# Kernel optimization log

Measured on AMD Instinct MI355X. Metric: run time of the kernel, lower is better.

## Reference

```python
import jax, jax.numpy as jnp
import numpy as np

DT = 0.01
OMEGA_MAX = 100.0


def setup_inputs() -> dict:
    key = jax.random.key(0)
    ks = jax.random.split(key, 7)
    B, T, D, M = 4, 4096, 1024, 64
    N = 2 * M
    u = jax.random.normal(ks[0], (B, T, D), dtype=jnp.float32)
    W_omega = jax.random.normal(ks[1], (M, D), dtype=jnp.float32) * 0.02
    b_omega = jnp.ones((M,), dtype=jnp.float32)
    W_zeta = jax.random.normal(ks[2], (M, D), dtype=jnp.float32) * 0.02
    b_zeta = jnp.zeros((M,), dtype=jnp.float32)
    W_B = jax.random.normal(ks[3], (N, D), dtype=jnp.float32) * (0.1 / np.sqrt(D))
    b_B = jnp.zeros((N,), dtype=jnp.float32)
    C = jax.random.normal(ks[4], (D, N), dtype=jnp.float32) * 0.01
    D_mat = jax.random.normal(ks[5], (D, D), dtype=jnp.float32) * 0.01
    return dict(u=u, W_omega=W_omega, b_omega=b_omega, W_zeta=W_zeta,
                b_zeta=b_zeta, W_B=W_B, b_B=b_B, C=C, D_mat=D_mat)


def reference(u, W_omega, b_omega, W_zeta, b_zeta, W_B, b_B, C, D_mat):
    B, T, D = u.shape
    M = W_omega.shape[0]
    # Hoist all per-step linear projections into batched GEMMs (same math).
    omega = jax.nn.softplus(jnp.einsum('btd,md->btm', u, W_omega) + b_omega)
    omega = jnp.clip(omega, 1e-4, OMEGA_MAX)                      # (B,T,M)
    zeta = jax.nn.sigmoid(jnp.einsum('btd,md->btm', u, W_zeta) + b_zeta)
    A = omega * omega                                             # (B,T,M)
    S = 1.0 / (1.0 + (DT * DT) * A)                               # (B,T,M)
    d = 1.0 - zeta                                                # (B,T,M)
    F = jnp.einsum('btd,nd->btn', u, W_B) + b_B                   # (B,T,2M)

    def step(x, inp):
        A_t, S_t, d_t, F_t = inp                                  # (B,M)x3, (B,2M)
        z = x[:, :M]
        y = x[:, M:]
        z_new = d_t * (S_t * z - DT * A_t * S_t * y)
        y_new = d_t * (DT * S_t * z + S_t * y)
        x_new = jnp.concatenate([z_new, y_new], axis=-1) + F_t
        return x_new, x_new

    x0 = jnp.zeros((B, 2 * M), dtype=u.dtype)
    tm = lambda a: jnp.swapaxes(a, 0, 1)  # to time-major for scan
    _, xs = jax.lax.scan(step, x0, (tm(A), tm(S), tm(d), tm(F)))
    xs = jnp.swapaxes(xs, 0, 1)                                   # (B,T,2M)
    # Output projection: y_t = x_t C^T + u_t D^T
    y = jnp.einsum('btn,dn->btd', xs, C) + jnp.einsum('bte,de->btd', u, D_mat)
    return y
```

## Files before the change

kernel.cpp:

```cpp
#include <hip/hip_runtime.h>
#include <hip/hip_bf16.h>
#include <math.h>

#define DTC 0.01f

typedef __attribute__((ext_vector_type(8))) short short8;
typedef __attribute__((ext_vector_type(4))) float f32x4;
typedef unsigned short bf16raw;

__device__ __forceinline__ bf16raw f2bf(float f){
  union { unsigned u; float f; } v; v.f = f;
  unsigned r = v.u + 0x7FFF + ((v.u >> 16) & 1u);
  return (bf16raw)(r >> 16);
}

__device__ __forceinline__ short8 ld8f(const float* __restrict__ p){
  float4 a = *(const float4*)p;
  float4 b = *(const float4*)(p + 4);
  short8 r;
  r[0] = (short)f2bf(a.x); r[1] = (short)f2bf(a.y);
  r[2] = (short)f2bf(a.z); r[3] = (short)f2bf(a.w);
  r[4] = (short)f2bf(b.x); r[5] = (short)f2bf(b.y);
  r[6] = (short)f2bf(b.z); r[7] = (short)f2bf(b.w);
  return r;
}

template<int ITERS>
__device__ __forceinline__ void stage_async(const bf16raw* __restrict__ src, long ld,
                                            long row0, int k0, bf16raw* lds,
                                            int wave, int lane){
#pragma unroll
  for (int i = 0; i < ITERS; ++i){
    int r0 = (wave*ITERS + i) * 16;
    long row = row0 + r0 + (lane >> 2);
    const bf16raw* gp = src + row*ld + k0 + (lane & 3)*8;
    bf16raw* lp = lds + r0*32;
    __builtin_amdgcn_global_load_lds((const __attribute__((address_space(1))) void*)gp,
                                     (__attribute__((address_space(3))) void*)lp,
                                     16, 0, 0);
  }
}

template<int NI>
__device__ __forceinline__ void mma_tile(const bf16raw* Alds, const bf16raw* Blds,
                                         f32x4 acc[4][NI], int wm, int wn, int quad, int t16){
  short8 af[4], bfr[NI];
#pragma unroll
  for (int mi = 0; mi < 4; ++mi)
    af[mi] = *(const short8*)(Alds + (wm*64 + mi*16 + t16)*32 + quad*8);
#pragma unroll
  for (int ni = 0; ni < NI; ++ni)
    bfr[ni] = *(const short8*)(Blds + (wn*(NI*16) + ni*16 + t16)*32 + quad*8);
#pragma unroll
  for (int mi = 0; mi < 4; ++mi)
#pragma unroll
    for (int ni = 0; ni < NI; ++ni)
      acc[mi][ni] = __builtin_amdgcn_mfma_f32_16x16x32_bf16(af[mi], bfr[ni], acc[mi][ni], 0, 0, 0);
}

extern "C" __global__ void k_prep(const float* __restrict__ u,
    const float* __restrict__ Wom, const float* __restrict__ Wze,
    const float* __restrict__ WB, const float* __restrict__ Cm,
    const float* __restrict__ Dm, bf16raw* __restrict__ u_bf,
    bf16raw* __restrict__ Wcat, bf16raw* __restrict__ C_bf,
    bf16raw* __restrict__ Dm_bf){
  long g = (long)blockIdx.x * 256 + threadIdx.x;
  const float* src; bf16raw* dst; long o;
  if      (g < 2097152){ src = u;   dst = u_bf;          o = g; }
  else if (g < 2105344){ src = Wom; dst = Wcat;          o = g - 2097152; }
  else if (g < 2113536){ src = Wze; dst = Wcat + 65536;  o = g - 2105344; }
  else if (g < 2129920){ src = WB;  dst = Wcat + 131072; o = g - 2113536; }
  else if (g < 2146304){ src = Cm;  dst = C_bf;          o = g - 2129920; }
  else                 { src = Dm;  dst = Dm_bf;         o = g - 2146304; }
  *(short8*)(dst + o*8) = ld8f(src + o*8);
}

extern "C" __global__ __launch_bounds__(256) void k_gemm_p(
    const bf16raw* __restrict__ u_bf, const bf16raw* __restrict__ Wcat,
    float* __restrict__ P){
  __shared__ __align__(16) bf16raw Alds[128*32];
  __shared__ __align__(16) bf16raw Blds[128*32];
  int tid = threadIdx.x, wave = tid >> 6, lane = tid & 63;
  int quad = lane >> 4, t16 = lane & 15;
  int wm = wave >> 1, wn = wave & 1;
  long row0 = (long)blockIdx.y * 128;
  int  col0 = blockIdx.x * 128;
  f32x4 acc[4][4] = {};
  for (int kt = 0; kt < 32; ++kt){
    __syncthreads();
    stage_async<2>(u_bf, 1024, row0, kt*32, Alds, wave, lane);
    stage_async<2>(Wcat, 1024, col0, kt*32, Blds, wave, lane);
    __syncthreads();
    mma_tile<4>(Alds, Blds, acc, wm, wn, quad, t16);
  }
#pragma unroll
  for (int mi = 0; mi < 4; ++mi)
#pragma unroll
    for (int ni = 0; ni < 4; ++ni)
#pragma unroll
      for (int r = 0; r < 4; ++r){
        long grow = row0 + wm*64 + mi*16 + quad*4 + r;
        int  gcol = col0 + wn*64 + ni*16 + t16;
        P[grow*256 + gcol] = acc[mi][ni][r];
      }
}

extern "C" __global__ __launch_bounds__(256, 2) void k_gemm_out(
    const bf16raw* __restrict__ Xs, const bf16raw* __restrict__ u_bf,
    const bf16raw* __restrict__ C_bf, const bf16raw* __restrict__ Dm_bf,
    float* __restrict__ out){
  __shared__ __align__(16) bf16raw Alds[128*32];
  __shared__ __align__(16) bf16raw Blds[256*32];
  int tid = threadIdx.x, wave = tid >> 6, lane = tid & 63;
  int quad = lane >> 4, t16 = lane & 15;
  int wm = wave >> 1, wn = wave & 1;
  long row0 = (long)blockIdx.y * 128;
  int  col0 = blockIdx.x * 256;
  f32x4 acc[4][8] = {};
  for (int kt = 0; kt < 4; ++kt){
    __syncthreads();
    stage_async<2>(Xs,   128, row0, kt*32, Alds, wave, lane);
    stage_async<4>(C_bf, 128, col0, kt*32, Blds, wave, lane);
    __syncthreads();
    mma_tile<8>(Alds, Blds, acc, wm, wn, quad, t16);
  }
  for (int kt = 0; kt < 32; ++kt){
    __syncthreads();
    stage_async<2>(u_bf,  1024, row0, kt*32, Alds, wave, lane);
    stage_async<4>(Dm_bf, 1024, col0, kt*32, Blds, wave, lane);
    __syncthreads();
    mma_tile<8>(Alds, Blds, acc, wm, wn, quad, t16);
  }
#pragma unroll
  for (int mi = 0; mi < 4; ++mi)
#pragma unroll
    for (int ni = 0; ni < 8; ++ni)
#pragma unroll
      for (int r = 0; r < 4; ++r){
        long grow = row0 + wm*64 + mi*16 + quad*4 + r;
        int  gcol = col0 + wn*128 + ni*16 + t16;
        out[grow*1024 + gcol] = acc[mi][ni][r];
      }
}

extern "C" __global__ void k_coef(const float* __restrict__ P,
    const float* __restrict__ b_om, const float* __restrict__ b_ze,
    const float* __restrict__ b_B, float4* __restrict__ Coef){
  int idx = blockIdx.x * 256 + threadIdx.x;
  int bt = idx >> 6, m = idx & 63;
  const float* row = P + (size_t)bt * 256;
  float wo = row[m]       + b_om[m];
  float wz = row[64 + m]  + b_ze[m];
  float fz = row[128 + m] + b_B[m];
  float fy = row[192 + m] + b_B[64 + m];
  float sp = (wo > 20.f) ? wo : log1pf(expf(wo));
  float omega = fminf(fmaxf(sp, 1e-4f), 100.f);
  float A = omega * omega;
  float S = 1.f / (1.f + DTC*DTC*A);
  float zeta = 1.f / (1.f + expf(-wz));
  float d = 1.f - zeta;
  float p = d * S;
  float q = p * DTC * A;
  Coef[idx] = make_float4(p, q, fz, fy);
}

extern "C" __global__ void k_scan1(const float4* __restrict__ Coef,
    float4* __restrict__ CM, float2* __restrict__ CV){
  int tid = threadIdx.x, c = blockIdx.x;
  int b = tid >> 6, m = tid & 63;
  const float4* cf = Coef + ((size_t)b*4096 + c*32)*64 + m;
  float m00=1.f, m01=0.f, m10=0.f, m11=0.f, vz=0.f, vy=0.f;
#pragma unroll 4
  for (int t = 0; t < 32; ++t){
    float4 f = cf[t*64];
    float p = f.x, q = f.y;
    float nvz = p*vz - q*vy + f.z;
    float nvy = DTC*p*vz + p*vy + f.w;
    vz = nvz; vy = nvy;
    float n00 = p*m00 - q*m10;
    float n01 = p*m01 - q*m11;
    float n10 = DTC*p*m00 + p*m10;
    float n11 = DTC*p*m01 + p*m11;
    m00=n00; m01=n01; m10=n10; m11=n11;
  }
  CM[c*256 + tid] = make_float4(m00, m01, m10, m11);
  CV[c*256 + tid] = make_float2(vz, vy);
}

extern "C" __global__ void k_scan2(const float4* __restrict__ CM,
    const float2* __restrict__ CV, float2* __restrict__ XIn){
  int tid = threadIdx.x;
  float xz = 0.f, xy = 0.f;
#pragma unroll 4
  for (int c = 0; c < 128; ++c){
    XIn[c*256 + tid] = make_float2(xz, xy);
    float4 Mv = CM[c*256 + tid];
    float2 Vv = CV[c*256 + tid];
    float nz = Mv.x*xz + Mv.y*xy + Vv.x;
    float ny = Mv.z*xz + Mv.w*xy + Vv.y;
    xz = nz; xy = ny;
  }
}

extern "C" __global__ void k_scan3(const float4* __restrict__ Coef,
    const float2* __restrict__ XIn, bf16raw* __restrict__ Xs){
  int tid = threadIdx.x, c = blockIdx.x;
  int b = tid >> 6, m = tid & 63;
  const float4* cf = Coef + ((size_t)b*4096 + c*32)*64 + m;
  float2 x0 = XIn[c*256 + tid];
  float xz = x0.x, xy = x0.y;
  bf16raw* xp = Xs + ((size_t)b*4096 + c*32)*128 + m;
#pragma unroll 4
  for (int t = 0; t < 32; ++t){
    float4 f = cf[t*64];
    float p = f.x, q = f.y;
    float nz = p*xz - q*xy + f.z;
    float ny = DTC*p*xz + p*xy + f.w;
    xz = nz; xy = ny;
    xp[t*128]      = f2bf(xz);
    xp[t*128 + 64] = f2bf(xy);
  }
}

extern "C" void kernel_launch(void* const* d_in, const int* in_sizes, int n_in,
                              void* d_out, int out_size, void* d_ws, size_t ws_size,
                              hipStream_t stream){
  const float* u   = (const float*)d_in[0];
  const float* Wom = (const float*)d_in[1];
  const float* bom = (const float*)d_in[2];
  const float* Wze = (const float*)d_in[3];
  const float* bze = (const float*)d_in[4];
  const float* WB  = (const float*)d_in[5];
  const float* bB  = (const float*)d_in[6];
  const float* Cm  = (const float*)d_in[7];
  const float* Dm  = (const float*)d_in[8];
  float* out = (float*)d_out;

  char* ws = (char*)d_ws;
  size_t off = 0;
  bf16raw* u_bf  = (bf16raw*)(ws + off); off += (size_t)16777216*2;
  bf16raw* Wcat  = (bf16raw*)(ws + off); off += (size_t)262144*2;
  bf16raw* C_bf  = (bf16raw*)(ws + off); off += (size_t)131072*2;
  bf16raw* Dm_bf = (bf16raw*)(ws + off); off += (size_t)1048576*2;
  float*   P     = (float*)  (ws + off);
  bf16raw* Xs    = (bf16raw*)P;
  off += (size_t)16384*256*4;
  float4*  Coef  = (float4*) (ws + off); off += (size_t)16384*64*16;
  float4*  CMw   = (float4*) (ws + off); off += (size_t)128*256*16;
  float2*  CVw   = (float2*) (ws + off); off += (size_t)128*256*8;
  float2*  XIn   = (float2*) (ws + off); off += (size_t)128*256*8;

  k_prep    <<<8896, 256, 0, stream>>>(u, Wom, Wze, WB, Cm, Dm, u_bf, Wcat, C_bf, Dm_bf);
  k_gemm_p  <<<dim3(2, 128), 256, 0, stream>>>(u_bf, Wcat, P);
  k_coef    <<<4096, 256, 0, stream>>>(P, bom, bze, bB, Coef);
  k_scan1   <<<128, 256, 0, stream>>>(Coef, CMw, CVw);
  k_scan2   <<<1, 256, 0, stream>>>(CMw, CVw, XIn);
  k_scan3   <<<128, 256, 0, stream>>>(Coef, XIn, Xs);
  k_gemm_out<<<dim3(4, 128), 256, 0, stream>>>(Xs, u_bf, C_bf, Dm_bf, out);
}
```

Baseline: 236.3 us.

## Double-buffer GEMM LDS tiles, swizzle block order, fuse coef into scan and drop serial carry

Both GEMMs now double-buffer their LDS tiles, prefetching the next K slice while the current one is multiplied, and raise wave priority around the MFMA work. Blocks are remapped in a grouped order to improve L2 reuse. The coefficient kernel is fused into the first scan pass, chunk size drops to 16 steps to give 256 blocks, and the single-block carry scan is removed. Each block of the final pass instead recomputes its starting state from all earlier chunk summaries, so the serial launch goes away at the cost of redundant work that grows with chunk index.

```diff
diff --git a/kernel.cpp b/kernel.cpp
--- a/kernel.cpp
+++ b/kernel.cpp
@@ -78,21 +78,35 @@
 extern "C" __global__ __launch_bounds__(256) void k_gemm_p(
     const bf16raw* __restrict__ u_bf, const bf16raw* __restrict__ Wcat,
     float* __restrict__ P){
-  __shared__ __align__(16) bf16raw Alds[128*32];
-  __shared__ __align__(16) bf16raw Blds[128*32];
+  __shared__ __align__(16) bf16raw Alds[2][128*32];
+  __shared__ __align__(16) bf16raw Blds[2][128*32];
   int tid = threadIdx.x, wave = tid >> 6, lane = tid & 63;
   int quad = lane >> 4, t16 = lane & 15;
   int wm = wave >> 1, wn = wave & 1;
-  long row0 = (long)blockIdx.y * 128;
-  int  col0 = blockIdx.x * 128;
+  int id  = blockIdx.y * gridDim.x + blockIdx.x;
+  int sid = (id & 7) * 32 + (id >> 3);
+  long row0 = (long)(sid >> 1) * 128;
+  int  col0 = (sid & 1) * 128;
   f32x4 acc[4][4] = {};
-  for (int kt = 0; kt < 32; ++kt){
-    __syncthreads();
-    stage_async<2>(u_bf, 1024, row0, kt*32, Alds, wave, lane);
-    stage_async<2>(Wcat, 1024, col0, kt*32, Blds, wave, lane);
-    __syncthreads();
-    mma_tile<4>(Alds, Blds, acc, wm, wn, quad, t16);
-  }
+
+  stage_async<2>(u_bf, 1024, row0, 0, Alds[0], wave, lane);
+  stage_async<2>(Wcat, 1024, col0, 0, Blds[0], wave, lane);
+  asm volatile("s_waitcnt vmcnt(0)" ::: "memory");
+  __builtin_amdgcn_s_barrier();
+  __builtin_amdgcn_sched_barrier(0);
+  int cur = 0;
+  for (int kt = 0; kt < 31; ++kt){
+    stage_async<2>(u_bf, 1024, row0, (kt+1)*32, Alds[cur^1], wave, lane);
+    stage_async<2>(Wcat, 1024, col0, (kt+1)*32, Blds[cur^1], wave, lane);
+    __builtin_amdgcn_s_setprio(1);
+    mma_tile<4>(Alds[cur], Blds[cur], acc, wm, wn, quad, t16);
+    __builtin_amdgcn_s_setprio(0);
+    asm volatile("s_waitcnt vmcnt(0)" ::: "memory");
+    __builtin_amdgcn_s_barrier();
+    __builtin_amdgcn_sched_barrier(0);
+    cur ^= 1;
+  }
+  mma_tile<4>(Alds[cur], Blds[cur], acc, wm, wn, quad, t16);
 #pragma unroll
   for (int mi = 0; mi < 4; ++mi)
 #pragma unroll
@@ -109,28 +123,43 @@
     const bf16raw* __restrict__ Xs, const bf16raw* __restrict__ u_bf,
     const bf16raw* __restrict__ C_bf, const bf16raw* __restrict__ Dm_bf,
     float* __restrict__ out){
-  __shared__ __align__(16) bf16raw Alds[128*32];
-  __shared__ __align__(16) bf16raw Blds[256*32];
+  __shared__ __align__(16) bf16raw Alds[2][128*32];
+  __shared__ __align__(16) bf16raw Blds[2][256*32];
   int tid = threadIdx.x, wave = tid >> 6, lane = tid & 63;
   int quad = lane >> 4, t16 = lane & 15;
   int wm = wave >> 1, wn = wave & 1;
-  long row0 = (long)blockIdx.y * 128;
-  int  col0 = blockIdx.x * 256;
+  int id  = blockIdx.y * gridDim.x + blockIdx.x;
+  int sid = (id & 7) * 64 + (id >> 3);
+  long row0 = (long)(sid >> 2) * 128;
+  int  col0 = (sid & 3) * 256;
   f32x4 acc[4][8] = {};
-  for (int kt = 0; kt < 4; ++kt){
-    __syncthreads();
-    stage_async<2>(Xs,   128, row0, kt*32, Alds, wave, lane);
-    stage_async<4>(C_bf, 128, col0, kt*32, Blds, wave, lane);
-    __syncthreads();
-    mma_tile<8>(Alds, Blds, acc, wm, wn, quad, t16);
-  }
-  for (int kt = 0; kt < 32; ++kt){
-    __syncthreads();
-    stage_async<2>(u_bf,  1024, row0, kt*32, Alds, wave, lane);
-    stage_async<4>(Dm_bf, 1024, col0, kt*32, Blds, wave, lane);
-    __syncthreads();
-    mma_tile<8>(Alds, Blds, acc, wm, wn, quad, t16);
-  }
+
+  auto stage = [&](int s, int buf){
+    if (s < 4){
+      stage_async<2>(Xs,   128, row0, s*32, Alds[buf], wave, lane);
+      stage_async<4>(C_bf, 128, col0, s*32, Blds[buf], wave, lane);
+    } else {
+      stage_async<2>(u_bf,  1024, row0, (s-4)*32, Alds[buf], wave, lane);
+      stage_async<4>(Dm_bf, 1024, col0, (s-4)*32, Blds[buf], wave, lane);
+    }
+  };
+
+  stage(0, 0);
+  asm volatile("s_waitcnt vmcnt(0)" ::: "memory");
+  __builtin_amdgcn_s_barrier();
+  __builtin_amdgcn_sched_barrier(0);
+  int cur = 0;
+  for (int s = 0; s < 35; ++s){
+    stage(s+1, cur^1);
+    __builtin_amdgcn_s_setprio(1);
+    mma_tile<8>(Alds[cur], Blds[cur], acc, wm, wn, quad, t16);
+    __builtin_amdgcn_s_setprio(0);
+    asm volatile("s_waitcnt vmcnt(0)" ::: "memory");
+    __builtin_amdgcn_s_barrier();
+    __builtin_amdgcn_sched_barrier(0);
+    cur ^= 1;
+  }
+  mma_tile<8>(Alds[cur], Blds[cur], acc, wm, wn, quad, t16);
 #pragma unroll
   for (int mi = 0; mi < 4; ++mi)
 #pragma unroll
@@ -143,39 +172,33 @@
       }
 }
 
-extern "C" __global__ void k_coef(const float* __restrict__ P,
-    const float* __restrict__ b_om, const float* __restrict__ b_ze,
-    const float* __restrict__ b_B, float4* __restrict__ Coef){
-  int idx = blockIdx.x * 256 + threadIdx.x;
-  int bt = idx >> 6, m = idx & 63;
-  const float* row = P + (size_t)bt * 256;
-  float wo = row[m]       + b_om[m];
-  float wz = row[64 + m]  + b_ze[m];
-  float fz = row[128 + m] + b_B[m];
-  float fy = row[192 + m] + b_B[64 + m];
-  float sp = (wo > 20.f) ? wo : log1pf(expf(wo));
-  float omega = fminf(fmaxf(sp, 1e-4f), 100.f);
-  float A = omega * omega;
-  float S = 1.f / (1.f + DTC*DTC*A);
-  float zeta = 1.f / (1.f + expf(-wz));
-  float d = 1.f - zeta;
-  float p = d * S;
-  float q = p * DTC * A;
-  Coef[idx] = make_float4(p, q, fz, fy);
-}
-
-extern "C" __global__ void k_scan1(const float4* __restrict__ Coef,
-    float4* __restrict__ CM, float2* __restrict__ CV){
+extern "C" __global__ __launch_bounds__(256) void k_scanA(
+    const float* __restrict__ P, const float* __restrict__ b_om,
+    const float* __restrict__ b_ze, const float* __restrict__ b_B,
+    float4* __restrict__ Coef, float4* __restrict__ CM, float2* __restrict__ CV){
   int tid = threadIdx.x, c = blockIdx.x;
   int b = tid >> 6, m = tid & 63;
-  const float4* cf = Coef + ((size_t)b*4096 + c*32)*64 + m;
+  float bo = b_om[m], bz = b_ze[m], bb0 = b_B[m], bb1 = b_B[64 + m];
+  const float* row = P + ((size_t)b*4096 + c*16) * 256;
+  float4* cf = Coef + ((size_t)b*4096 + c*16) * 64 + m;
   float m00=1.f, m01=0.f, m10=0.f, m11=0.f, vz=0.f, vy=0.f;
 #pragma unroll 4
-  for (int t = 0; t < 32; ++t){
-    float4 f = cf[t*64];
-    float p = f.x, q = f.y;
-    float nvz = p*vz - q*vy + f.z;
-    float nvy = DTC*p*vz + p*vy + f.w;
+  for (int t = 0; t < 16; ++t){
+    const float* r = row + t*256;
+    float wo = r[m]       + bo;
+    float wz = r[64 + m]  + bz;
+    float fz = r[128 + m] + bb0;
+    float fy = r[192 + m] + bb1;
+    float sp = (wo > 20.f) ? wo : log1pf(expf(wo));
+    float omega = fminf(fmaxf(sp, 1e-4f), 100.f);
+    float A = omega * omega;
+    float S = 1.f / (1.f + DTC*DTC*A);
+    float zeta = 1.f / (1.f + expf(-wz));
+    float p = (1.f - zeta) * S;
+    float q = p * DTC * A;
+    cf[t*64] = make_float4(p, q, fz, fy);
+    float nvz = p*vz - q*vy + fz;
+    float nvy = DTC*p*vz + p*vy + fy;
     vz = nvz; vy = nvy;
     float n00 = p*m00 - q*m10;
     float n01 = p*m01 - q*m11;
@@ -187,35 +210,27 @@
   CV[c*256 + tid] = make_float2(vz, vy);
 }
 
-extern "C" __global__ void k_scan2(const float4* __restrict__ CM,
-    const float2* __restrict__ CV, float2* __restrict__ XIn){
-  int tid = threadIdx.x;
+extern "C" __global__ __launch_bounds__(256) void k_scanC(
+    const float4* __restrict__ Coef, const float4* __restrict__ CM,
+    const float2* __restrict__ CV, bf16raw* __restrict__ Xs){
+  int tid = threadIdx.x, c = blockIdx.x;
+  int b = tid >> 6, m = tid & 63;
   float xz = 0.f, xy = 0.f;
 #pragma unroll 4
-  for (int c = 0; c < 128; ++c){
-    XIn[c*256 + tid] = make_float2(xz, xy);
-    float4 Mv = CM[c*256 + tid];
-    float2 Vv = CV[c*256 + tid];
+  for (int j = 0; j < c; ++j){
+    float4 Mv = CM[j*256 + tid];
+    float2 Vv = CV[j*256 + tid];
     float nz = Mv.x*xz + Mv.y*xy + Vv.x;
     float ny = Mv.z*xz + Mv.w*xy + Vv.y;
     xz = nz; xy = ny;
   }
-}
-
-extern "C" __global__ void k_scan3(const float4* __restrict__ Coef,
-    const float2* __restrict__ XIn, bf16raw* __restrict__ Xs){
-  int tid = threadIdx.x, c = blockIdx.x;
-  int b = tid >> 6, m = tid & 63;
-  const float4* cf = Coef + ((size_t)b*4096 + c*32)*64 + m;
-  float2 x0 = XIn[c*256 + tid];
-  float xz = x0.x, xy = x0.y;
-  bf16raw* xp = Xs + ((size_t)b*4096 + c*32)*128 + m;
+  const float4* cf = Coef + ((size_t)b*4096 + c*16) * 64 + m;
+  bf16raw* xp = Xs + ((size_t)b*4096 + c*16) * 128 + m;
 #pragma unroll 4
-  for (int t = 0; t < 32; ++t){
+  for (int t = 0; t < 16; ++t){
     float4 f = cf[t*64];
-    float p = f.x, q = f.y;
-    float nz = p*xz - q*xy + f.z;
-    float ny = DTC*p*xz + p*xy + f.w;
+    float nz = f.x*xz - f.y*xy + f.z;
+    float ny = DTC*f.x*xz + f.x*xy + f.w;
     xz = nz; xy = ny;
     xp[t*128]      = f2bf(xz);
     xp[t*128 + 64] = f2bf(xy);
@@ -246,15 +261,12 @@
   bf16raw* Xs    = (bf16raw*)P;
   off += (size_t)16384*256*4;
   float4*  Coef  = (float4*) (ws + off); off += (size_t)16384*64*16;
-  float4*  CMw   = (float4*) (ws + off); off += (size_t)128*256*16;
-  float2*  CVw   = (float2*) (ws + off); off += (size_t)128*256*8;
-  float2*  XIn   = (float2*) (ws + off); off += (size_t)128*256*8;
+  float4*  CMw   = (float4*) (ws + off); off += (size_t)256*256*16;
+  float2*  CVw   = (float2*) (ws + off); off += (size_t)256*256*8;
 
   k_prep    <<<8896, 256, 0, stream>>>(u, Wom, Wze, WB, Cm, Dm, u_bf, Wcat, C_bf, Dm_bf);
   k_gemm_p  <<<dim3(2, 128), 256, 0, stream>>>(u_bf, Wcat, P);
-  k_coef    <<<4096, 256, 0, stream>>>(P, bom, bze, bB, Coef);
-  k_scan1   <<<128, 256, 0, stream>>>(Coef, CMw, CVw);
-  k_scan2   <<<1, 256, 0, stream>>>(CMw, CVw, XIn);
-  k_scan3   <<<128, 256, 0, stream>>>(Coef, XIn, Xs);
+  k_scanA   <<<256, 256, 0, stream>>>(P, bom, bze, bB, Coef, CMw, CVw);
+  k_scanC   <<<256, 256, 0, stream>>>(Coef, CMw, CVw, Xs);
   k_gemm_out<<<dim3(4, 128), 256, 0, stream>>>(Xs, u_bf, C_bf, Dm_bf, out);
 }
```

Result: no change. 240.5 us (+1.8%).
